# Kernel optimization log

Measured on AMD Instinct MI355X. Metric: run time of the kernel, lower is better.

The kernel has to match this reference:

```python
import jax, jax.numpy as jnp
import numpy as np

HEADS = 4
HID = 256
MAX_OFFSET = 2


def setup_inputs() -> dict:
    key = jax.random.key(0)
    ks = jax.random.split(key, 8)
    B, T, C = 4, 512, HID
    x = jax.random.normal(ks[0], (B, T, C), jnp.float32)
    mask = jax.random.randint(ks[1], (B, 1, T), 0, 2).astype(bool)
    s2 = 1.0 / np.sqrt(2 * C)
    s1 = 1.0 / np.sqrt(C)
    W_subj = jax.random.uniform(ks[2], (2 * C, C), jnp.float32, -s2, s2)
    b_subj = jax.random.uniform(ks[3], (C,), jnp.float32, -s2, s2)
    W_obj = jax.random.uniform(ks[4], (2 * C, C), jnp.float32, -s2, s2)
    b_obj = jax.random.uniform(ks[5], (C,), jnp.float32, -s2, s2)
    W_t = jax.random.uniform(ks[6], (C, HEADS), jnp.float32, -s1, s1)
    b_t = jax.random.uniform(ks[7], (HEADS,), jnp.float32, -s1, s1)
    return {"x": x, "W_subj": W_subj, "b_subj": b_subj, "W_obj": W_obj,
            "b_obj": b_obj, "W_t": W_t, "b_t": b_t, "mask": mask}


def reference(x, W_subj, b_subj, W_obj, b_obj, W_t, b_t, mask):
    # x: [B,T,C]. torch MaxPool1d on [B,T,C] pools over the LAST dim (C),
    # kernel = 2*MAX_OFFSET+1, stride 1, same padding (pad value -inf).
    k = 2 * MAX_OFFSET + 1
    x_pooled = jax.lax.reduce_window(
        x, -jnp.inf, jax.lax.max,
        window_dimensions=(1, 1, k), window_strides=(1, 1, 1),
        padding=[(0, 0), (0, 0), (MAX_OFFSET, MAX_OFFSET)])
    x_new = jnp.concatenate([x_pooled, x], axis=2)      # [B,T,2C]
    subj = x_new @ W_subj + b_subj                      # [B,T,C]
    obj = x_new @ W_obj + b_obj                         # [B,T,C]
    # subj.unsqueeze(1): varies over axis 2; obj.unsqueeze(2): varies over axis 1
    abs_multi = jnp.abs(subj[:, None, :, :] - obj[:, :, None, :])  # [B,T,T,C]
    rep = abs_multi @ W_t + b_t                         # [B,T,T,H]
    attn = jax.nn.softmax(jax.nn.relu(rep), axis=2)     # softmax over obj axis
    m = mask[:, 0, :]                                   # [B,T]
    mm = m[:, None, :] & m[:, :, None]                  # [B,T,T]
    attn = jnp.where(mm[..., None], 0.0, attn)          # masked_fill -> 0
    return x_new, attn  # attn[..., h] == attn_adj_list[h]
```

## Files before the change

kernel.cpp:

```cpp
#include <hip/hip_runtime.h>
#include <hip/hip_bf16.h>
#include <math.h>

#define NB 4
#define NT 512
#define NC 256
#define NC2 512
#define NH 4

__global__ void k_mask(const unsigned char* __restrict__ raw, int* __restrict__ out) {
    __shared__ int s_bytes;
    if (threadIdx.x == 0) s_bytes = 0;
    __syncthreads();
    int flag = 0;
    const unsigned* w = (const unsigned*)raw;
    for (int i = threadIdx.x; i < (NB * NT) / 4; i += blockDim.x)
        if (w[i] > 1u) flag = 1;
    if (flag) atomicOr(&s_bytes, 1);
    __syncthreads();
    const int ib = s_bytes;
    for (int i = threadIdx.x; i < NB * NT; i += blockDim.x) {
        int v = ib ? (int)raw[i] : ((const int*)raw)[i];
        out[i] = v ? 1 : 0;
    }
}

__global__ __launch_bounds__(512) void k_poolproj(
    const float* __restrict__ x,
    const float* __restrict__ Ws, const float* __restrict__ bs,
    const float* __restrict__ Wo, const float* __restrict__ bo,
    float* __restrict__ xnew,
    float* __restrict__ subj, float* __restrict__ obj) {
    const int r0 = blockIdx.x * 8;
    const int tid = threadIdx.x;
    __shared__ float xraw[8][260];
    __shared__ float xp[8][260];
    __shared__ float xt[NC2][12];
    __shared__ float red[256][17];

    {
        int r = tid >> 6, c4 = tid & 63;
        float4 v = *(const float4*)(x + ((size_t)(r0 + r)) * NC + c4 * 4);
        *(float4*)&xraw[r][c4 * 4] = v;
    }
    __syncthreads();
#pragma unroll
    for (int p = 0; p < 4; ++p) {
        int u = p * 512 + tid;
        int r = u >> 8, c = u & 255;
        float m = xraw[r][c];
        if (c >= 1) m = fmaxf(m, xraw[r][c - 1]);
        if (c >= 2) m = fmaxf(m, xraw[r][c - 2]);
        if (c <= 254) m = fmaxf(m, xraw[r][c + 1]);
        if (c <= 253) m = fmaxf(m, xraw[r][c + 2]);
        xp[r][c] = m;
    }
    __syncthreads();
#pragma unroll
    for (int p = 0; p < 2; ++p) {
        int idx = p * 512 + tid;
        int r = idx & 7, k4 = idx >> 3;
        float4 v = (k4 < 64) ? *(const float4*)&xp[r][k4 * 4]
                             : *(const float4*)&xraw[r][(k4 - 64) * 4];
        xt[k4 * 4 + 0][r] = v.x; xt[k4 * 4 + 1][r] = v.y;
        xt[k4 * 4 + 2][r] = v.z; xt[k4 * 4 + 3][r] = v.w;
    }
#pragma unroll
    for (int p = 0; p < 2; ++p) {
        int u = p * 512 + tid;
        int r = u >> 7, k4 = u & 127;
        float4 v = (k4 < 64) ? *(const float4*)&xp[r][k4 * 4]
                             : *(const float4*)&xraw[r][(k4 - 64) * 4];
        *(float4*)(xnew + ((size_t)(r0 + r)) * NC2 + k4 * 4) = v;
    }
    __syncthreads();

    const int c = tid & 255;
    const int kh = tid >> 8;
    const int kbase = kh * 256;

    float acs[8], aco[8];
#pragma unroll
    for (int r = 0; r < 8; ++r) { acs[r] = 0.f; aco[r] = 0.f; }

    const float* wsp = Ws + (size_t)kbase * NC + c;
    const float* wop = Wo + (size_t)kbase * NC + c;
    float wsb[8], wob[8];
#pragma unroll
    for (int q = 0; q < 8; ++q) { wsb[q] = wsp[q * NC]; wob[q] = wop[q * NC]; }

    for (int kk = 0; kk < 256; kk += 8) {
        float wsn[8], won[8];
        if (kk + 8 < 256) {
#pragma unroll
            for (int q = 0; q < 8; ++q) {
                wsn[q] = wsp[(kk + 8 + q) * NC];
                won[q] = wop[(kk + 8 + q) * NC];
            }
        }
#pragma unroll
        for (int q = 0; q < 8; ++q) {
            float4 xa = *(const float4*)&xt[kbase + kk + q][0];
            float4 xb = *(const float4*)&xt[kbase + kk + q][4];
            float ws = wsb[q], wo = wob[q];
            acs[0] = fmaf(xa.x, ws, acs[0]); aco[0] = fmaf(xa.x, wo, aco[0]);
            acs[1] = fmaf(xa.y, ws, acs[1]); aco[1] = fmaf(xa.y, wo, aco[1]);
            acs[2] = fmaf(xa.z, ws, acs[2]); aco[2] = fmaf(xa.z, wo, aco[2]);
            acs[3] = fmaf(xa.w, ws, acs[3]); aco[3] = fmaf(xa.w, wo, aco[3]);
            acs[4] = fmaf(xb.x, ws, acs[4]); aco[4] = fmaf(xb.x, wo, aco[4]);
            acs[5] = fmaf(xb.y, ws, acs[5]); aco[5] = fmaf(xb.y, wo, aco[5]);
            acs[6] = fmaf(xb.z, ws, acs[6]); aco[6] = fmaf(xb.z, wo, aco[6]);
            acs[7] = fmaf(xb.w, ws, acs[7]); aco[7] = fmaf(xb.w, wo, aco[7]);
        }
#pragma unroll
        for (int q = 0; q < 8; ++q) { wsb[q] = wsn[q]; wob[q] = won[q]; }
    }

    if (kh == 1) {
#pragma unroll
        for (int q = 0; q < 8; ++q) { red[c][q] = acs[q]; red[c][8 + q] = aco[q]; }
    }
    __syncthreads();
    if (kh == 0) {
        const float bsv = bs[c], bov = bo[c];
#pragma unroll
        for (int r = 0; r < 8; ++r) {
            subj[(size_t)(r0 + r) * NC + c] = acs[r] + red[c][r] + bsv;
            obj[(size_t)(r0 + r) * NC + c]  = aco[r] + red[c][8 + r] + bov;
        }
    }
}

#define OFS(r) ((r) * 68 + ((r) >> 2) * 4)
#define OFO(r) ((r) * 36 + ((r) >> 2) * 4)
__global__ __launch_bounds__(256) void k_rep(
    const float* __restrict__ subj, const float* __restrict__ obj,
    const float* __restrict__ Wt, const float* __restrict__ bt,
    float* __restrict__ attn) {
    const int bx = blockIdx.x;
    const int b = bx >> 7;
    const int rem = bx & 127;
    const int it = rem >> 3, jt = rem & 7;
    const int i0 = it * 32, j0 = jt * 64;

    __shared__ float sjT[4416];
    __shared__ float obT[2368];

    const int tid = threadIdx.x;
    const int tx = tid & 15;
    const int ty = tid >> 4;

    const float4* WtV = (const float4*)Wt;

    float acc[2][4][4];
#pragma unroll
    for (int ii = 0; ii < 2; ++ii)
#pragma unroll
        for (int jj = 0; jj < 4; ++jj)
#pragma unroll
            for (int h = 0; h < 4; ++h) acc[ii][jj][h] = 0.f;

    for (int cc = 0; cc < NC; cc += 64) {
        if (cc) __syncthreads();
#pragma unroll
        for (int p = 0; p < 4; ++p) {
            int u = p * 256 + tid;
            int j = u >> 4, c4 = u & 15;
            float4 vs = *(const float4*)(subj + ((size_t)(b * NT) + j0 + j) * NC + cc + c4 * 4);
            int rb = c4 * 4;
            sjT[OFS(rb + 0) + j] = vs.x;
            sjT[OFS(rb + 1) + j] = vs.y;
            sjT[OFS(rb + 2) + j] = vs.z;
            sjT[OFS(rb + 3) + j] = vs.w;
        }
#pragma unroll
        for (int p = 0; p < 2; ++p) {
            int u = p * 256 + tid;
            int i = u >> 4, c4 = u & 15;
            float4 vo = *(const float4*)(obj + ((size_t)(b * NT) + i0 + i) * NC + cc + c4 * 4);
            int rb = c4 * 4;
            obT[OFO(rb + 0) + i] = vo.x;
            obT[OFO(rb + 1) + i] = vo.y;
            obT[OFO(rb + 2) + i] = vo.z;
            obT[OFO(rb + 3) + i] = vo.w;
        }
        __syncthreads();

#pragma unroll 4
        for (int cl = 0; cl < 64; ++cl) {
            float4 s4 = *(const float4*)&sjT[OFS(cl) + tx * 4];
            float2 o2 = *(const float2*)&obT[OFO(cl) + ty * 2];
            float4 w4 = WtV[cc + cl];
            float sv[4] = {s4.x, s4.y, s4.z, s4.w};
            float ov[2] = {o2.x, o2.y};
#pragma unroll
            for (int ii = 0; ii < 2; ++ii)
#pragma unroll
                for (int jj = 0; jj < 4; ++jj) {
                    float d = fabsf(sv[jj] - ov[ii]);
                    acc[ii][jj][0] = fmaf(d, w4.x, acc[ii][jj][0]);
                    acc[ii][jj][1] = fmaf(d, w4.y, acc[ii][jj][1]);
                    acc[ii][jj][2] = fmaf(d, w4.z, acc[ii][jj][2]);
                    acc[ii][jj][3] = fmaf(d, w4.w, acc[ii][jj][3]);
                }
        }
    }

    const float4 btv = *(const float4*)bt;
#pragma unroll
    for (int ii = 0; ii < 2; ++ii) {
        const int i = i0 + ty * 2 + ii;
#pragma unroll
        for (int jj = 0; jj < 4; ++jj) {
            const int j = j0 + tx * 4 + jj;
            float4 r;
            r.x = fmaxf(acc[ii][jj][0] + btv.x, 0.f);
            r.y = fmaxf(acc[ii][jj][1] + btv.y, 0.f);
            r.z = fmaxf(acc[ii][jj][2] + btv.z, 0.f);
            r.w = fmaxf(acc[ii][jj][3] + btv.w, 0.f);
            *(float4*)&attn[(((size_t)b * NT + i) * NT + j) * NH] = r;
        }
    }
}

__global__ void k_soft(float* __restrict__ attn, const int* __restrict__ mask) {
    const int bi = blockIdx.x;
    const int b = bi >> 9;
    float4* row = (float4*)(attn + (size_t)bi * (NT * NH));
    const int t = threadIdx.x;
    float4 v0 = row[t];
    float4 v1 = row[t + 256];

    float mx[4] = {fmaxf(v0.x, v1.x), fmaxf(v0.y, v1.y),
                   fmaxf(v0.z, v1.z), fmaxf(v0.w, v1.w)};
#pragma unroll
    for (int off = 32; off; off >>= 1) {
#pragma unroll
        for (int h = 0; h < 4; ++h) mx[h] = fmaxf(mx[h], __shfl_xor(mx[h], off));
    }
    __shared__ float redm[4][4], reds[4][4];
    const int wid = t >> 6, lane = t & 63;
    if (lane == 0) {
#pragma unroll
        for (int h = 0; h < 4; ++h) redm[wid][h] = mx[h];
    }
    __syncthreads();
#pragma unroll
    for (int h = 0; h < 4; ++h)
        mx[h] = fmaxf(fmaxf(redm[0][h], redm[1][h]), fmaxf(redm[2][h], redm[3][h]));

    float e0[4] = {expf(v0.x - mx[0]), expf(v0.y - mx[1]),
                   expf(v0.z - mx[2]), expf(v0.w - mx[3])};
    float e1[4] = {expf(v1.x - mx[0]), expf(v1.y - mx[1]),
                   expf(v1.z - mx[2]), expf(v1.w - mx[3])};
    float sm[4] = {e0[0] + e1[0], e0[1] + e1[1], e0[2] + e1[2], e0[3] + e1[3]};
#pragma unroll
    for (int off = 32; off; off >>= 1) {
#pragma unroll
        for (int h = 0; h < 4; ++h) sm[h] += __shfl_xor(sm[h], off);
    }
    if (lane == 0) {
#pragma unroll
        for (int h = 0; h < 4; ++h) reds[wid][h] = sm[h];
    }
    __syncthreads();
    float rinv[4];
#pragma unroll
    for (int h = 0; h < 4; ++h)
        rinv[h] = 1.0f / (reds[0][h] + reds[1][h] + reds[2][h] + reds[3][h]);

    const int mi = mask[bi];
    const int mj0 = mask[b * NT + t];
    const int mj1 = mask[b * NT + t + 256];
    float4 o0, o1;
    o0.x = (mi & mj0) ? 0.f : e0[0] * rinv[0];
    o0.y = (mi & mj0) ? 0.f : e0[1] * rinv[1];
    o0.z = (mi & mj0) ? 0.f : e0[2] * rinv[2];
    o0.w = (mi & mj0) ? 0.f : e0[3] * rinv[3];
    o1.x = (mi & mj1) ? 0.f : e1[0] * rinv[0];
    o1.y = (mi & mj1) ? 0.f : e1[1] * rinv[1];
    o1.z = (mi & mj1) ? 0.f : e1[2] * rinv[2];
    o1.w = (mi & mj1) ? 0.f : e1[3] * rinv[3];
    row[t] = o0;
    row[t + 256] = o1;
}

extern "C" void kernel_launch(void* const* d_in, const int* in_sizes, int n_in,
                              void* d_out, int out_size, void* d_ws, size_t ws_size,
                              hipStream_t stream) {
    const float* x      = (const float*)d_in[0];
    const float* W_subj = (const float*)d_in[1];
    const float* b_subj = (const float*)d_in[2];
    const float* W_obj  = (const float*)d_in[3];
    const float* b_obj  = (const float*)d_in[4];
    const float* W_t    = (const float*)d_in[5];
    const float* b_t    = (const float*)d_in[6];
    const unsigned char* mask_raw = (const unsigned char*)d_in[7];

    float* xnew = (float*)d_out;
    float* attn = xnew + (size_t)NB * NT * NC2;

    int* wmask  = (int*)d_ws;
    float* subj = (float*)d_ws + NB * NT;
    float* obj  = subj + (size_t)NB * NT * NC;

    hipLaunchKernelGGL(k_mask, dim3(1), dim3(256), 0, stream, mask_raw, wmask);
    hipLaunchKernelGGL(k_poolproj, dim3(NB * NT / 8), dim3(512), 0, stream,
                       x, W_subj, b_subj, W_obj, b_obj, xnew, subj, obj);
    hipLaunchKernelGGL(k_rep, dim3(NB * 16 * 8), dim3(256), 0, stream,
                       subj, obj, W_t, b_t, attn);
    hipLaunchKernelGGL(k_soft, dim3(NB * NT), dim3(256), 0, stream, attn, wmask);
}
```

Baseline: 162.9 us.

## Restructure projection GEMM to float4 column tiles with tree reduction and prefetch Wt

The projection kernel now gives each thread 4 output columns (float4 weight loads) over a 64-wide K slice, using 8 K-groups instead of 2. Partial sums are combined through a shared-memory tree reduction, and shared memory is aliased into a single buffer. In the pairwise rep kernel, the inner loop is manually unrolled with double-buffered prefetch of Wt rows into registers to hide load latency. This adds register pressure and several extra barriers in exchange for wider loads and more ILP.

```diff
diff --git a/kernel.cpp b/kernel.cpp
--- a/kernel.cpp
+++ b/kernel.cpp
@@ -33,10 +33,10 @@
     float* __restrict__ subj, float* __restrict__ obj) {
     const int r0 = blockIdx.x * 8;
     const int tid = threadIdx.x;
-    __shared__ float xraw[8][260];
-    __shared__ float xp[8][260];
-    __shared__ float xt[NC2][12];
-    __shared__ float red[256][17];
+    __shared__ float smem[10560];
+    float (*xraw)[260] = (float (*)[260])smem;
+    float (*xp)[260]   = (float (*)[260])(smem + 2080);
+    float (*xt)[12]    = (float (*)[12])(smem + 4160);
 
     {
         int r = tid >> 6, c4 = tid & 63;
@@ -75,58 +75,105 @@
     }
     __syncthreads();
 
-    const int c = tid & 255;
-    const int kh = tid >> 8;
-    const int kbase = kh * 256;
-
-    float acs[8], aco[8];
-#pragma unroll
-    for (int r = 0; r < 8; ++r) { acs[r] = 0.f; aco[r] = 0.f; }
-
-    const float* wsp = Ws + (size_t)kbase * NC + c;
-    const float* wop = Wo + (size_t)kbase * NC + c;
-    float wsb[8], wob[8];
-#pragma unroll
-    for (int q = 0; q < 8; ++q) { wsb[q] = wsp[q * NC]; wob[q] = wop[q * NC]; }
-
-    for (int kk = 0; kk < 256; kk += 8) {
-        float wsn[8], won[8];
-        if (kk + 8 < 256) {
-#pragma unroll
-            for (int q = 0; q < 8; ++q) {
-                wsn[q] = wsp[(kk + 8 + q) * NC];
-                won[q] = wop[(kk + 8 + q) * NC];
+    const int c4 = tid & 63;
+    const int kh = tid >> 6;
+    const int kbase = kh * 64;
+
+    float4 as[8], ao[8];
+#pragma unroll
+    for (int r = 0; r < 8; ++r) {
+        as[r] = make_float4(0.f, 0.f, 0.f, 0.f);
+        ao[r] = make_float4(0.f, 0.f, 0.f, 0.f);
+    }
+
+    const float4* WsV = (const float4*)Ws + (size_t)kbase * 64 + c4;
+    const float4* WoV = (const float4*)Wo + (size_t)kbase * 64 + c4;
+
+    float4 wsA, woA, xaA, xbA, wsB, woB, xaB, xbB;
+    wsA = WsV[0]; woA = WoV[0];
+    xaA = *(const float4*)&xt[kbase][0];
+    xbA = *(const float4*)&xt[kbase][4];
+
+#define FMA8(WS, WO, XA, XB) { \
+    const float xv0 = XA.x, xv1 = XA.y, xv2 = XA.z, xv3 = XA.w; \
+    const float xv4 = XB.x, xv5 = XB.y, xv6 = XB.z, xv7 = XB.w; \
+    as[0].x=fmaf(xv0,WS.x,as[0].x); as[0].y=fmaf(xv0,WS.y,as[0].y); as[0].z=fmaf(xv0,WS.z,as[0].z); as[0].w=fmaf(xv0,WS.w,as[0].w); \
+    ao[0].x=fmaf(xv0,WO.x,ao[0].x); ao[0].y=fmaf(xv0,WO.y,ao[0].y); ao[0].z=fmaf(xv0,WO.z,ao[0].z); ao[0].w=fmaf(xv0,WO.w,ao[0].w); \
+    as[1].x=fmaf(xv1,WS.x,as[1].x); as[1].y=fmaf(xv1,WS.y,as[1].y); as[1].z=fmaf(xv1,WS.z,as[1].z); as[1].w=fmaf(xv1,WS.w,as[1].w); \
+    ao[1].x=fmaf(xv1,WO.x,ao[1].x); ao[1].y=fmaf(xv1,WO.y,ao[1].y); ao[1].z=fmaf(xv1,WO.z,ao[1].z); ao[1].w=fmaf(xv1,WO.w,ao[1].w); \
+    as[2].x=fmaf(xv2,WS.x,as[2].x); as[2].y=fmaf(xv2,WS.y,as[2].y); as[2].z=fmaf(xv2,WS.z,as[2].z); as[2].w=fmaf(xv2,WS.w,as[2].w); \
+    ao[2].x=fmaf(xv2,WO.x,ao[2].x); ao[2].y=fmaf(xv2,WO.y,ao[2].y); ao[2].z=fmaf(xv2,WO.z,ao[2].z); ao[2].w=fmaf(xv2,WO.w,ao[2].w); \
+    as[3].x=fmaf(xv3,WS.x,as[3].x); as[3].y=fmaf(xv3,WS.y,as[3].y); as[3].z=fmaf(xv3,WS.z,as[3].z); as[3].w=fmaf(xv3,WS.w,as[3].w); \
+    ao[3].x=fmaf(xv3,WO.x,ao[3].x); ao[3].y=fmaf(xv3,WO.y,ao[3].y); ao[3].z=fmaf(xv3,WO.z,ao[3].z); ao[3].w=fmaf(xv3,WO.w,ao[3].w); \
+    as[4].x=fmaf(xv4,WS.x,as[4].x); as[4].y=fmaf(xv4,WS.y,as[4].y); as[4].z=fmaf(xv4,WS.z,as[4].z); as[4].w=fmaf(xv4,WS.w,as[4].w); \
+    ao[4].x=fmaf(xv4,WO.x,ao[4].x); ao[4].y=fmaf(xv4,WO.y,ao[4].y); ao[4].z=fmaf(xv4,WO.z,ao[4].z); ao[4].w=fmaf(xv4,WO.w,ao[4].w); \
+    as[5].x=fmaf(xv5,WS.x,as[5].x); as[5].y=fmaf(xv5,WS.y,as[5].y); as[5].z=fmaf(xv5,WS.z,as[5].z); as[5].w=fmaf(xv5,WS.w,as[5].w); \
+    ao[5].x=fmaf(xv5,WO.x,ao[5].x); ao[5].y=fmaf(xv5,WO.y,ao[5].y); ao[5].z=fmaf(xv5,WO.z,ao[5].z); ao[5].w=fmaf(xv5,WO.w,ao[5].w); \
+    as[6].x=fmaf(xv6,WS.x,as[6].x); as[6].y=fmaf(xv6,WS.y,as[6].y); as[6].z=fmaf(xv6,WS.z,as[6].z); as[6].w=fmaf(xv6,WS.w,as[6].w); \
+    ao[6].x=fmaf(xv6,WO.x,ao[6].x); ao[6].y=fmaf(xv6,WO.y,ao[6].y); ao[6].z=fmaf(xv6,WO.z,ao[6].z); ao[6].w=fmaf(xv6,WO.w,ao[6].w); \
+    as[7].x=fmaf(xv7,WS.x,as[7].x); as[7].y=fmaf(xv7,WS.y,as[7].y); as[7].z=fmaf(xv7,WS.z,as[7].z); as[7].w=fmaf(xv7,WS.w,as[7].w); \
+    ao[7].x=fmaf(xv7,WO.x,ao[7].x); ao[7].y=fmaf(xv7,WO.y,ao[7].y); ao[7].z=fmaf(xv7,WO.z,ao[7].z); ao[7].w=fmaf(xv7,WO.w,ao[7].w); }
+
+#define PPSTEP(K, WSC, WOC, XAC, XBC, WSN, WON, XAN, XBN) { \
+    const int kn = ((K) + 1) & 63; \
+    WSN = WsV[(size_t)kn * 64]; WON = WoV[(size_t)kn * 64]; \
+    XAN = *(const float4*)&xt[kbase + kn][0]; \
+    XBN = *(const float4*)&xt[kbase + kn][4]; \
+    FMA8(WSC, WOC, XAC, XBC) }
+
+    for (int k = 0; k < 64; k += 2) {
+        PPSTEP(k,     wsA, woA, xaA, xbA, wsB, woB, xaB, xbB)
+        PPSTEP(k + 1, wsB, woB, xaB, xbB, wsA, woA, xaA, xbA)
+    }
+#undef PPSTEP
+#undef FMA8
+
+    __syncthreads();
+    float4* rb4 = (float4*)smem;
+    for (int half = 4; half >= 1; half >>= 1) {
+        if (kh >= half && kh < 2 * half) {
+            float4* d = rb4 + (kh - half) * 64 + c4;
+#pragma unroll
+            for (int r = 0; r < 8; ++r) d[r * 256] = as[r];
+        }
+        __syncthreads();
+        if (kh < half) {
+            const float4* s = rb4 + kh * 64 + c4;
+#pragma unroll
+            for (int r = 0; r < 8; ++r) {
+                float4 v = s[r * 256];
+                as[r].x += v.x; as[r].y += v.y; as[r].z += v.z; as[r].w += v.w;
             }
         }
-#pragma unroll
-        for (int q = 0; q < 8; ++q) {
-            float4 xa = *(const float4*)&xt[kbase + kk + q][0];
-            float4 xb = *(const float4*)&xt[kbase + kk + q][4];
-            float ws = wsb[q], wo = wob[q];
-            acs[0] = fmaf(xa.x, ws, acs[0]); aco[0] = fmaf(xa.x, wo, aco[0]);
-            acs[1] = fmaf(xa.y, ws, acs[1]); aco[1] = fmaf(xa.y, wo, aco[1]);
-            acs[2] = fmaf(xa.z, ws, acs[2]); aco[2] = fmaf(xa.z, wo, aco[2]);
-            acs[3] = fmaf(xa.w, ws, acs[3]); aco[3] = fmaf(xa.w, wo, aco[3]);
-            acs[4] = fmaf(xb.x, ws, acs[4]); aco[4] = fmaf(xb.x, wo, aco[4]);
-            acs[5] = fmaf(xb.y, ws, acs[5]); aco[5] = fmaf(xb.y, wo, aco[5]);
-            acs[6] = fmaf(xb.z, ws, acs[6]); aco[6] = fmaf(xb.z, wo, aco[6]);
-            acs[7] = fmaf(xb.w, ws, acs[7]); aco[7] = fmaf(xb.w, wo, aco[7]);
-        }
-#pragma unroll
-        for (int q = 0; q < 8; ++q) { wsb[q] = wsn[q]; wob[q] = won[q]; }
-    }
-
-    if (kh == 1) {
-#pragma unroll
-        for (int q = 0; q < 8; ++q) { red[c][q] = acs[q]; red[c][8 + q] = aco[q]; }
-    }
-    __syncthreads();
+        __syncthreads();
+        if (kh >= half && kh < 2 * half) {
+            float4* d = rb4 + (kh - half) * 64 + c4;
+#pragma unroll
+            for (int r = 0; r < 8; ++r) d[r * 256] = ao[r];
+        }
+        __syncthreads();
+        if (kh < half) {
+            const float4* s = rb4 + kh * 64 + c4;
+#pragma unroll
+            for (int r = 0; r < 8; ++r) {
+                float4 v = s[r * 256];
+                ao[r].x += v.x; ao[r].y += v.y; ao[r].z += v.z; ao[r].w += v.w;
+            }
+        }
+        __syncthreads();
+    }
+
     if (kh == 0) {
-        const float bsv = bs[c], bov = bo[c];
+        float4 bsv = ((const float4*)bs)[c4];
+        float4 bov = ((const float4*)bo)[c4];
 #pragma unroll
         for (int r = 0; r < 8; ++r) {
-            subj[(size_t)(r0 + r) * NC + c] = acs[r] + red[c][r] + bsv;
-            obj[(size_t)(r0 + r) * NC + c]  = aco[r] + red[c][8 + r] + bov;
+            float4 vs = make_float4(as[r].x + bsv.x, as[r].y + bsv.y,
+                                    as[r].z + bsv.z, as[r].w + bsv.w);
+            float4 vo = make_float4(ao[r].x + bov.x, ao[r].y + bov.y,
+                                    ao[r].z + bov.z, ao[r].w + bov.w);
+            *(float4*)&subj[(size_t)(r0 + r) * NC + c4 * 4] = vs;
+            *(float4*)&obj[(size_t)(r0 + r) * NC + c4 * 4]  = vo;
         }
     }
 }
@@ -160,14 +207,53 @@
 #pragma unroll
             for (int h = 0; h < 4; ++h) acc[ii][jj][h] = 0.f;
 
+#define FMABLK(Q, W4) { \
+    const int cl = g4 + (Q); \
+    const float4 s4 = *(const float4*)&sjT[OFS(cl) + tx * 4]; \
+    const float2 o2 = *(const float2*)&obT[OFO(cl) + ty * 2]; \
+    const float sv0 = s4.x, sv1 = s4.y, sv2 = s4.z, sv3 = s4.w; \
+    const float ov0 = o2.x, ov1 = o2.y; \
+    float d; \
+    d = sv0 - ov0; \
+    acc[0][0][0]=fmaf(fabsf(d),W4.x,acc[0][0][0]); acc[0][0][1]=fmaf(fabsf(d),W4.y,acc[0][0][1]); \
+    acc[0][0][2]=fmaf(fabsf(d),W4.z,acc[0][0][2]); acc[0][0][3]=fmaf(fabsf(d),W4.w,acc[0][0][3]); \
+    d = sv1 - ov0; \
+    acc[0][1][0]=fmaf(fabsf(d),W4.x,acc[0][1][0]); acc[0][1][1]=fmaf(fabsf(d),W4.y,acc[0][1][1]); \
+    acc[0][1][2]=fmaf(fabsf(d),W4.z,acc[0][1][2]); acc[0][1][3]=fmaf(fabsf(d),W4.w,acc[0][1][3]); \
+    d = sv2 - ov0; \
+    acc[0][2][0]=fmaf(fabsf(d),W4.x,acc[0][2][0]); acc[0][2][1]=fmaf(fabsf(d),W4.y,acc[0][2][1]); \
+    acc[0][2][2]=fmaf(fabsf(d),W4.z,acc[0][2][2]); acc[0][2][3]=fmaf(fabsf(d),W4.w,acc[0][2][3]); \
+    d = sv3 - ov0; \
+    acc[0][3][0]=fmaf(fabsf(d),W4.x,acc[0][3][0]); acc[0][3][1]=fmaf(fabsf(d),W4.y,acc[0][3][1]); \
+    acc[0][3][2]=fmaf(fabsf(d),W4.z,acc[0][3][2]); acc[0][3][3]=fmaf(fabsf(d),W4.w,acc[0][3][3]); \
+    d = sv0 - ov1; \
+    acc[1][0][0]=fmaf(fabsf(d),W4.x,acc[1][0][0]); acc[1][0][1]=fmaf(fabsf(d),W4.y,acc[1][0][1]); \
+    acc[1][0][2]=fmaf(fabsf(d),W4.z,acc[1][0][2]); acc[1][0][3]=fmaf(fabsf(d),W4.w,acc[1][0][3]); \
+    d = sv1 - ov1; \
+    acc[1][1][0]=fmaf(fabsf(d),W4.x,acc[1][1][0]); acc[1][1][1]=fmaf(fabsf(d),W4.y,acc[1][1][1]); \
+    acc[1][1][2]=fmaf(fabsf(d),W4.z,acc[1][1][2]); acc[1][1][3]=fmaf(fabsf(d),W4.w,acc[1][1][3]); \
+    d = sv2 - ov1; \
+    acc[1][2][0]=fmaf(fabsf(d),W4.x,acc[1][2][0]); acc[1][2][1]=fmaf(fabsf(d),W4.y,acc[1][2][1]); \
+    acc[1][2][2]=fmaf(fabsf(d),W4.z,acc[1][2][2]); acc[1][2][3]=fmaf(fabsf(d),W4.w,acc[1][2][3]); \
+    d = sv3 - ov1; \
+    acc[1][3][0]=fmaf(fabsf(d),W4.x,acc[1][3][0]); acc[1][3][1]=fmaf(fabsf(d),W4.y,acc[1][3][1]); \
+    acc[1][3][2]=fmaf(fabsf(d),W4.z,acc[1][3][2]); acc[1][3][3]=fmaf(fabsf(d),W4.w,acc[1][3][3]); }
+
+#define GSTEP(G, WC0, WC1, WC2, WC3, WN0, WN1, WN2, WN3) { \
+    const int gn = ((G) + 1) & 15; \
+    WN0 = WtV[cc + gn * 4 + 0]; WN1 = WtV[cc + gn * 4 + 1]; \
+    WN2 = WtV[cc + gn * 4 + 2]; WN3 = WtV[cc + gn * 4 + 3]; \
+    const int g4 = (G) * 4; \
+    FMABLK(0, WC0) FMABLK(1, WC1) FMABLK(2, WC2) FMABLK(3, WC3) }
+
     for (int cc = 0; cc < NC; cc += 64) {
         if (cc) __syncthreads();
 #pragma unroll
         for (int p = 0; p < 4; ++p) {
             int u = p * 256 + tid;
-            int j = u >> 4, c4 = u & 15;
-            float4 vs = *(const float4*)(subj + ((size_t)(b * NT) + j0 + j) * NC + cc + c4 * 4);
-            int rb = c4 * 4;
+            int j = u >> 4, c4s = u & 15;
+            float4 vs = *(const float4*)(subj + ((size_t)(b * NT) + j0 + j) * NC + cc + c4s * 4);
+            int rb = c4s * 4;
             sjT[OFS(rb + 0) + j] = vs.x;
             sjT[OFS(rb + 1) + j] = vs.y;
             sjT[OFS(rb + 2) + j] = vs.z;
@@ -176,9 +262,9 @@
 #pragma unroll
         for (int p = 0; p < 2; ++p) {
             int u = p * 256 + tid;
-            int i = u >> 4, c4 = u & 15;
-            float4 vo = *(const float4*)(obj + ((size_t)(b * NT) + i0 + i) * NC + cc + c4 * 4);
-            int rb = c4 * 4;
+            int i = u >> 4, c4s = u & 15;
+            float4 vo = *(const float4*)(obj + ((size_t)(b * NT) + i0 + i) * NC + cc + c4s * 4);
+            int rb = c4s * 4;
             obT[OFO(rb + 0) + i] = vo.x;
             obT[OFO(rb + 1) + i] = vo.y;
             obT[OFO(rb + 2) + i] = vo.z;
@@ -186,25 +272,15 @@
         }
         __syncthreads();
 
-#pragma unroll 4
-        for (int cl = 0; cl < 64; ++cl) {
-            float4 s4 = *(const float4*)&sjT[OFS(cl) + tx * 4];
-            float2 o2 = *(const float2*)&obT[OFO(cl) + ty * 2];
-            float4 w4 = WtV[cc + cl];
-            float sv[4] = {s4.x, s4.y, s4.z, s4.w};
-            float ov[2] = {o2.x, o2.y};
-#pragma unroll
-            for (int ii = 0; ii < 2; ++ii)
-#pragma unroll
-                for (int jj = 0; jj < 4; ++jj) {
-                    float d = fabsf(sv[jj] - ov[ii]);
-                    acc[ii][jj][0] = fmaf(d, w4.x, acc[ii][jj][0]);
-                    acc[ii][jj][1] = fmaf(d, w4.y, acc[ii][jj][1]);
-                    acc[ii][jj][2] = fmaf(d, w4.z, acc[ii][jj][2]);
-                    acc[ii][jj][3] = fmaf(d, w4.w, acc[ii][jj][3]);
-                }
-        }
-    }
+        float4 w0A = WtV[cc + 0], w1A = WtV[cc + 1], w2A = WtV[cc + 2], w3A = WtV[cc + 3];
+        float4 w0B, w1B, w2B, w3B;
+        for (int g = 0; g < 16; g += 2) {
+            GSTEP(g,     w0A, w1A, w2A, w3A, w0B, w1B, w2B, w3B)
+            GSTEP(g + 1, w0B, w1B, w2B, w3B, w0A, w1A, w2A, w3A)
+        }
+    }
+#undef GSTEP
+#undef FMABLK
 
     const float4 btv = *(const float4*)bt;
 #pragma unroll
```

Result: slower. 170.2 us (+4.5%).
